# Kernel tuning notes

Measured on AMD Instinct MI355X. Metric: run time of the kernel, lower is better.

## Reference

```python
import jax, jax.numpy as jnp
import numpy as np

N_NODES = 100000
N_EDGES = 600000
D_IN = 128
D_OUT = 128


def setup_inputs() -> dict:
    key = jax.random.key(0)
    ks = jax.random.split(key, 8)
    stdv = 1.0 / np.sqrt(D_OUT)
    return {
        "x": jax.random.normal(ks[0], (N_NODES, D_IN), dtype=jnp.float32),
        "edge_src": jax.random.randint(ks[1], (N_EDGES,), 0, N_NODES, dtype=jnp.int32),
        "edge_dst": jax.random.randint(ks[2], (N_EDGES,), 0, N_NODES, dtype=jnp.int32),
        "edge_weight": jax.random.uniform(ks[3], (N_EDGES,), dtype=jnp.float32),
        "weight_l": jax.random.uniform(ks[4], (D_IN, D_OUT), minval=-stdv, maxval=stdv, dtype=jnp.float32),
        "bias_l": jax.random.uniform(ks[5], (D_OUT,), minval=-stdv, maxval=stdv, dtype=jnp.float32),
        "weight_r": jax.random.uniform(ks[6], (D_IN, D_OUT), minval=-stdv, maxval=stdv, dtype=jnp.float32),
        "bias_r": jax.random.uniform(ks[7], (D_OUT,), minval=-stdv, maxval=stdv, dtype=jnp.float32),
    }


def reference(x, edge_src, edge_dst, edge_weight, weight_l, bias_l, weight_r, bias_r):
    # h = input @ weight_l  -> [N, D_OUT]
    h = x @ weight_l
    # spmm(adj, h): out[dst] += adj[dst, src] * h[src]
    msgs = h[edge_src] * edge_weight[:, None]          # [E, D_OUT] gather
    agg = jax.ops.segment_sum(msgs, edge_dst, num_segments=N_NODES)
    out = agg + bias_l
    # root_weight branch (size is None)
    out = out + x @ weight_r + bias_r
    return out
```

## Files before the change

kernel.cpp:

```cpp
#include <hip/hip_runtime.h>
#include <hip/hip_bf16.h>

#define D 128
#define SCAN_BLK 256
#define SCAN_VPT 4
#define SCAN_TILE (SCAN_BLK * SCAN_VPT)

typedef __attribute__((ext_vector_type(8))) short short8;
typedef __attribute__((ext_vector_type(4))) float f32x4;

__global__ __launch_bounds__(256) void prep_w(
    const float* __restrict__ Wl, const float* __restrict__ Wr,
    const float* __restrict__ bl, const float* __restrict__ br,
    __hip_bfloat16* __restrict__ WTl, __hip_bfloat16* __restrict__ WTr,
    float* __restrict__ bsum) {
  const int tid = blockIdx.x * 256 + threadIdx.x;
  const int n = (tid >> 7) & 127;
  const int k = tid & 127;
  if (tid < 16384) {
    WTl[n * D + k] = __float2bfloat16(Wl[k * D + n]);
  } else {
    WTr[n * D + k] = __float2bfloat16(Wr[k * D + n]);
  }
  if (tid < 128) bsum[tid] = bl[tid] + br[tid];
}

__global__ __launch_bounds__(256) void gemm_mfma(
    const float* __restrict__ x,
    const __hip_bfloat16* __restrict__ WTl,
    const __hip_bfloat16* __restrict__ WTr,
    const float* __restrict__ bsum,
    __hip_bfloat16* __restrict__ h,
    float* __restrict__ out,
    int n_rowtiles) {
  __shared__ __hip_bfloat16 xs[16][136];
  const int t = threadIdx.x;
  const int wave = t >> 6;
  const int lane = t & 63;
  const int m = lane & 15;
  const int q = lane >> 4;

  const __hip_bfloat16* __restrict__ WT = (wave < 2) ? WTl : WTr;
  const int ctbase = (wave & 1) * 4;
  short8 bfrag[4][4];
#pragma unroll
  for (int ct = 0; ct < 4; ++ct) {
    const int n0 = (ctbase + ct) * 16;
#pragma unroll
    for (int ks = 0; ks < 4; ++ks)
      bfrag[ct][ks] = *(const short8*)&WT[(n0 + m) * D + ks * 32 + q * 8];
  }

  const int srow = t >> 4;
  const int scol = (t & 15) * 8;

  for (int rt = blockIdx.x; rt < n_rowtiles; rt += gridDim.x) {
    const int rowbase = rt * 16;
    {
      const float4* src = (const float4*)&x[(size_t)(rowbase + srow) * D + scol];
      const float4 v0 = src[0], v1 = src[1];
      __hip_bfloat16* dst = &xs[srow][scol];
      dst[0] = __float2bfloat16(v0.x); dst[1] = __float2bfloat16(v0.y);
      dst[2] = __float2bfloat16(v0.z); dst[3] = __float2bfloat16(v0.w);
      dst[4] = __float2bfloat16(v1.x); dst[5] = __float2bfloat16(v1.y);
      dst[6] = __float2bfloat16(v1.z); dst[7] = __float2bfloat16(v1.w);
    }
    __syncthreads();

    f32x4 acc[4];
#pragma unroll
    for (int ct = 0; ct < 4; ++ct)
#pragma unroll
      for (int r = 0; r < 4; ++r) acc[ct][r] = 0.f;

#pragma unroll
    for (int ks = 0; ks < 4; ++ks) {
      const short8 afrag = *(const short8*)&xs[m][ks * 32 + q * 8];
#pragma unroll
      for (int ct = 0; ct < 4; ++ct)
        acc[ct] = __builtin_amdgcn_mfma_f32_16x16x32_bf16(afrag, bfrag[ct][ks], acc[ct], 0, 0, 0);
    }

    if (wave < 2) {
#pragma unroll
      for (int ct = 0; ct < 4; ++ct) {
        const int n = (ctbase + ct) * 16 + m;
#pragma unroll
        for (int r = 0; r < 4; ++r)
          h[(size_t)(rowbase + q * 4 + r) * D + n] = __float2bfloat16(acc[ct][r]);
      }
    } else {
#pragma unroll
      for (int ct = 0; ct < 4; ++ct) {
        const int n = (ctbase + ct) * 16 + m;
        const float b = bsum[n];
#pragma unroll
        for (int r = 0; r < 4; ++r)
          out[(size_t)(rowbase + q * 4 + r) * D + n] = acc[ct][r] + b;
      }
    }
    __syncthreads();
  }
}

__global__ __launch_bounds__(256) void hist_kernel(
    const int* __restrict__ edst, int* __restrict__ deg, int n_edges) {
  const int e = blockIdx.x * 256 + threadIdx.x;
  if (e < n_edges) atomicAdd(&deg[edst[e]], 1);
}

__global__ __launch_bounds__(SCAN_BLK) void scan1_kernel(
    const int* __restrict__ deg, int* __restrict__ offsets,
    int* __restrict__ partials, int n) {
  __shared__ int sdata[SCAN_BLK];
  const int t = threadIdx.x;
  const int base = blockIdx.x * SCAN_TILE + t * SCAN_VPT;

  int v[SCAN_VPT];
  int s = 0;
#pragma unroll
  for (int j = 0; j < SCAN_VPT; ++j) {
    v[j] = (base + j < n) ? deg[base + j] : 0;
    s += v[j];
  }
  sdata[t] = s;
  __syncthreads();
  for (int off = 1; off < SCAN_BLK; off <<= 1) {
    int xv = (t >= off) ? sdata[t - off] : 0;
    __syncthreads();
    sdata[t] += xv;
    __syncthreads();
  }
  int excl = sdata[t] - s;
  if (t == SCAN_BLK - 1) partials[blockIdx.x] = sdata[t];
  int run = excl;
#pragma unroll
  for (int j = 0; j < SCAN_VPT; ++j) {
    if (base + j < n) offsets[base + j] = run;
    run += v[j];
  }
}

__global__ __launch_bounds__(128) void scan2_kernel(int* __restrict__ partials, int nparts) {
  __shared__ int sd[128];
  const int t = threadIdx.x;
  const int v = (t < nparts) ? partials[t] : 0;
  sd[t] = v;
  __syncthreads();
  for (int off = 1; off < 128; off <<= 1) {
    int xv = (t >= off) ? sd[t - off] : 0;
    __syncthreads();
    sd[t] += xv;
    __syncthreads();
  }
  if (t < nparts) partials[t] = sd[t] - v;
}

__global__ __launch_bounds__(SCAN_BLK) void scan3_kernel(
    int* __restrict__ offsets, int* __restrict__ pos,
    const int* __restrict__ partials, int n, int n_edges) {
  const int base = blockIdx.x * SCAN_TILE + threadIdx.x * SCAN_VPT;
  const int add = partials[blockIdx.x];
#pragma unroll
  for (int j = 0; j < SCAN_VPT; ++j) {
    const int i = base + j;
    if (i < n) {
      const int o = offsets[i] + add;
      offsets[i] = o;
      pos[i] = o;
    }
  }
  if (blockIdx.x == 0 && threadIdx.x == 0) offsets[n] = n_edges;
}

__global__ __launch_bounds__(256) void scatter_kernel(
    const int* __restrict__ esrc, const int* __restrict__ edst,
    const float* __restrict__ ew, int* __restrict__ pos,
    int2* __restrict__ pairs, int n_edges) {
  const int e = blockIdx.x * 256 + threadIdx.x;
  if (e >= n_edges) return;
  const int d = edst[e];
  const int slot = atomicAdd(&pos[d], 1);
  pairs[slot] = make_int2(esrc[e], __float_as_int(ew[e]));
}

__global__ __launch_bounds__(256) void aggregate_kernel(
    const __hip_bfloat16* __restrict__ h, const int* __restrict__ offsets,
    const int2* __restrict__ pairs, float* __restrict__ out, int n_nodes) {
  const int node = blockIdx.x * 4 + (threadIdx.x >> 6);
  if (node >= n_nodes) return;
  const int t = threadIdx.x & 63;
  const int begin = offsets[node];
  const int end = offsets[node + 1];
  const __hip_bfloat162* __restrict__ h2 = (const __hip_bfloat162*)h;

  float2 acc = *(const float2*)&out[(size_t)node * D + 2 * t];

  int i = begin;
  for (; i + 4 <= end; i += 4) {
    const int2 p0 = pairs[i + 0];
    const int2 p1 = pairs[i + 1];
    const int2 p2 = pairs[i + 2];
    const int2 p3 = pairs[i + 3];
    const __hip_bfloat162 a0 = h2[(size_t)p0.x * (D / 2) + t];
    const __hip_bfloat162 a1 = h2[(size_t)p1.x * (D / 2) + t];
    const __hip_bfloat162 a2 = h2[(size_t)p2.x * (D / 2) + t];
    const __hip_bfloat162 a3 = h2[(size_t)p3.x * (D / 2) + t];
    const float w0 = __int_as_float(p0.y), w1 = __int_as_float(p1.y);
    const float w2 = __int_as_float(p2.y), w3 = __int_as_float(p3.y);
    acc.x = fmaf(w0, __bfloat162float(a0.x), acc.x);
    acc.y = fmaf(w0, __bfloat162float(a0.y), acc.y);
    acc.x = fmaf(w1, __bfloat162float(a1.x), acc.x);
    acc.y = fmaf(w1, __bfloat162float(a1.y), acc.y);
    acc.x = fmaf(w2, __bfloat162float(a2.x), acc.x);
    acc.y = fmaf(w2, __bfloat162float(a2.y), acc.y);
    acc.x = fmaf(w3, __bfloat162float(a3.x), acc.x);
    acc.y = fmaf(w3, __bfloat162float(a3.y), acc.y);
  }
  for (; i < end; ++i) {
    const int2 p = pairs[i];
    const __hip_bfloat162 a = h2[(size_t)p.x * (D / 2) + t];
    const float w = __int_as_float(p.y);
    acc.x = fmaf(w, __bfloat162float(a.x), acc.x);
    acc.y = fmaf(w, __bfloat162float(a.y), acc.y);
  }
  *(float2*)&out[(size_t)node * D + 2 * t] = acc;
}

extern "C" void kernel_launch(void* const* d_in, const int* in_sizes, int n_in,
                              void* d_out, int out_size, void* d_ws, size_t ws_size,
                              hipStream_t stream) {
  const float* x   = (const float*)d_in[0];
  const int* esrc  = (const int*)d_in[1];
  const int* edst  = (const int*)d_in[2];
  const float* ew  = (const float*)d_in[3];
  const float* Wl  = (const float*)d_in[4];
  const float* bl  = (const float*)d_in[5];
  const float* Wr  = (const float*)d_in[6];
  const float* br  = (const float*)d_in[7];
  float* out = (float*)d_out;

  const int n_nodes = in_sizes[0] / D;
  const int n_edges = in_sizes[1];

  char* ws = (char*)d_ws;
  size_t off = 0;
  __hip_bfloat16* h = (__hip_bfloat16*)(ws + off);
  off += (size_t)n_nodes * D * sizeof(__hip_bfloat16);
  off = (off + 15) & ~15ull;
  int* offsets = (int*)(ws + off);
  off += (size_t)(n_nodes + 1) * sizeof(int);
  off = (off + 15) & ~15ull;
  int* pos = (int*)(ws + off);
  off += (size_t)n_nodes * sizeof(int);
  off = (off + 15) & ~15ull;
  int* partials = (int*)(ws + off);
  off += 1024 * sizeof(int);
  off = (off + 15) & ~15ull;
  int2* pairs = (int2*)(ws + off);
  off += (size_t)n_edges * sizeof(int2);
  off = (off + 15) & ~15ull;
  __hip_bfloat16* WTl = (__hip_bfloat16*)(ws + off);
  off += (size_t)D * D * sizeof(__hip_bfloat16);
  __hip_bfloat16* WTr = (__hip_bfloat16*)(ws + off);
  off += (size_t)D * D * sizeof(__hip_bfloat16);
  float* bsum = (float*)(ws + off);
  off += D * sizeof(float);

  prep_w<<<128, 256, 0, stream>>>(Wl, Wr, bl, br, WTl, WTr, bsum);
  const int n_rowtiles = (n_nodes + 15) / 16;
  const int gemm_grid = n_rowtiles < 2048 ? n_rowtiles : 2048;
  gemm_mfma<<<gemm_grid, 256, 0, stream>>>(x, WTl, WTr, bsum, h, out, n_rowtiles);

  hipMemsetAsync(pos, 0, (size_t)n_nodes * sizeof(int), stream);
  hist_kernel<<<(n_edges + 255) / 256, 256, 0, stream>>>(edst, pos, n_edges);
  const int nparts = (n_nodes + SCAN_TILE - 1) / SCAN_TILE;
  scan1_kernel<<<nparts, SCAN_BLK, 0, stream>>>(pos, offsets, partials, n_nodes);
  scan2_kernel<<<1, 128, 0, stream>>>(partials, nparts);
  scan3_kernel<<<nparts, SCAN_BLK, 0, stream>>>(offsets, pos, partials, n_nodes, n_edges);
  scatter_kernel<<<(n_edges + 255) / 256, 256, 0, stream>>>(esrc, edst, ew, pos, pairs, n_edges);

  aggregate_kernel<<<(n_nodes + 3) / 4, 256, 0, stream>>>(h, offsets, pairs, out, n_nodes);
}
```

Before: 251.0 us.

## Fuse histogram into h GEMM, root GEMM into aggregation, drop scan2

Runs the degree histogram inside the h GEMM kernel and drops the separate hist launch. The root-weight GEMM plus bias moves into the aggregation kernel, which stages it in shared memory, so out is written once instead of written then re-read and rewritten. scan2 is removed by having each scan3 block reduce its preceding partials itself. This saves launches and an N×D fp32 round trip, but the aggregation kernel now uses more shared memory, re-reads x, and assigns four nodes per wave sequentially, which may cut latency hiding. sage_out also has no bounds check, so it assumes n_nodes is a multiple of 16.

```diff
diff --git a/kernel.cpp b/kernel.cpp
--- a/kernel.cpp
+++ b/kernel.cpp
@@ -25,14 +25,15 @@
   if (tid < 128) bsum[tid] = bl[tid] + br[tid];
 }
 
-__global__ __launch_bounds__(256) void gemm_mfma(
-    const float* __restrict__ x,
-    const __hip_bfloat16* __restrict__ WTl,
-    const __hip_bfloat16* __restrict__ WTr,
-    const float* __restrict__ bsum,
+__global__ __launch_bounds__(256) void gemm_h(
+    const float* __restrict__ x, const __hip_bfloat16* __restrict__ WTl,
     __hip_bfloat16* __restrict__ h,
-    float* __restrict__ out,
+    const int* __restrict__ edst, int* __restrict__ deg, int n_edges,
     int n_rowtiles) {
+  const int gsz = gridDim.x * 256;
+  for (int e = blockIdx.x * 256 + threadIdx.x; e < n_edges; e += gsz)
+    atomicAdd(&deg[edst[e]], 1);
+
   __shared__ __hip_bfloat16 xs[16][136];
   const int t = threadIdx.x;
   const int wave = t >> 6;
@@ -40,15 +41,13 @@
   const int m = lane & 15;
   const int q = lane >> 4;
 
-  const __hip_bfloat16* __restrict__ WT = (wave < 2) ? WTl : WTr;
-  const int ctbase = (wave & 1) * 4;
-  short8 bfrag[4][4];
-#pragma unroll
-  for (int ct = 0; ct < 4; ++ct) {
-    const int n0 = (ctbase + ct) * 16;
+  short8 bfrag[2][4];
+#pragma unroll
+  for (int c = 0; c < 2; ++c) {
+    const int n0 = wave * 32 + c * 16;
 #pragma unroll
     for (int ks = 0; ks < 4; ++ks)
-      bfrag[ct][ks] = *(const short8*)&WT[(n0 + m) * D + ks * 32 + q * 8];
+      bfrag[c][ks] = *(const short8*)&WTl[(n0 + m) * D + ks * 32 + q * 8];
   }
 
   const int srow = t >> 4;
@@ -67,46 +66,29 @@
     }
     __syncthreads();
 
-    f32x4 acc[4];
-#pragma unroll
-    for (int ct = 0; ct < 4; ++ct)
-#pragma unroll
-      for (int r = 0; r < 4; ++r) acc[ct][r] = 0.f;
+    f32x4 acc[2];
+#pragma unroll
+    for (int c = 0; c < 2; ++c)
+#pragma unroll
+      for (int r = 0; r < 4; ++r) acc[c][r] = 0.f;
 
 #pragma unroll
     for (int ks = 0; ks < 4; ++ks) {
       const short8 afrag = *(const short8*)&xs[m][ks * 32 + q * 8];
 #pragma unroll
-      for (int ct = 0; ct < 4; ++ct)
-        acc[ct] = __builtin_amdgcn_mfma_f32_16x16x32_bf16(afrag, bfrag[ct][ks], acc[ct], 0, 0, 0);
-    }
-
-    if (wave < 2) {
-#pragma unroll
-      for (int ct = 0; ct < 4; ++ct) {
-        const int n = (ctbase + ct) * 16 + m;
-#pragma unroll
-        for (int r = 0; r < 4; ++r)
-          h[(size_t)(rowbase + q * 4 + r) * D + n] = __float2bfloat16(acc[ct][r]);
-      }
-    } else {
-#pragma unroll
-      for (int ct = 0; ct < 4; ++ct) {
-        const int n = (ctbase + ct) * 16 + m;
-        const float b = bsum[n];
-#pragma unroll
-        for (int r = 0; r < 4; ++r)
-          out[(size_t)(rowbase + q * 4 + r) * D + n] = acc[ct][r] + b;
-      }
+      for (int c = 0; c < 2; ++c)
+        acc[c] = __builtin_amdgcn_mfma_f32_16x16x32_bf16(afrag, bfrag[c][ks], acc[c], 0, 0, 0);
+    }
+
+#pragma unroll
+    for (int c = 0; c < 2; ++c) {
+      const int n = wave * 32 + c * 16 + m;
+#pragma unroll
+      for (int r = 0; r < 4; ++r)
+        h[(size_t)(rowbase + q * 4 + r) * D + n] = __float2bfloat16(acc[c][r]);
     }
     __syncthreads();
   }
-}
-
-__global__ __launch_bounds__(256) void hist_kernel(
-    const int* __restrict__ edst, int* __restrict__ deg, int n_edges) {
-  const int e = blockIdx.x * 256 + threadIdx.x;
-  if (e < n_edges) atomicAdd(&deg[edst[e]], 1);
 }
 
 __global__ __launch_bounds__(SCAN_BLK) void scan1_kernel(
@@ -141,26 +123,21 @@
   }
 }
 
-__global__ __launch_bounds__(128) void scan2_kernel(int* __restrict__ partials, int nparts) {
-  __shared__ int sd[128];
-  const int t = threadIdx.x;
-  const int v = (t < nparts) ? partials[t] : 0;
-  sd[t] = v;
-  __syncthreads();
-  for (int off = 1; off < 128; off <<= 1) {
-    int xv = (t >= off) ? sd[t - off] : 0;
-    __syncthreads();
-    sd[t] += xv;
-    __syncthreads();
-  }
-  if (t < nparts) partials[t] = sd[t] - v;
-}
-
 __global__ __launch_bounds__(SCAN_BLK) void scan3_kernel(
     int* __restrict__ offsets, int* __restrict__ pos,
     const int* __restrict__ partials, int n, int n_edges) {
-  const int base = blockIdx.x * SCAN_TILE + threadIdx.x * SCAN_VPT;
-  const int add = partials[blockIdx.x];
+  __shared__ int s_add;
+  const int t = threadIdx.x;
+  if (t < 64) {
+    int v = 0;
+    for (int j = t; j < blockIdx.x; j += 64) v += partials[j];
+#pragma unroll
+    for (int off = 32; off > 0; off >>= 1) v += __shfl_down(v, off);
+    if (t == 0) s_add = v;
+  }
+  __syncthreads();
+  const int add = s_add;
+  const int base = blockIdx.x * SCAN_TILE + t * SCAN_VPT;
 #pragma unroll
   for (int j = 0; j < SCAN_VPT; ++j) {
     const int i = base + j;
@@ -170,7 +147,7 @@
       pos[i] = o;
     }
   }
-  if (blockIdx.x == 0 && threadIdx.x == 0) offsets[n] = n_edges;
+  if (blockIdx.x == 0 && t == 0) offsets[n] = n_edges;
 }
 
 __global__ __launch_bounds__(256) void scatter_kernel(
@@ -184,47 +161,106 @@
   pairs[slot] = make_int2(esrc[e], __float_as_int(ew[e]));
 }
 
-__global__ __launch_bounds__(256) void aggregate_kernel(
-    const __hip_bfloat16* __restrict__ h, const int* __restrict__ offsets,
-    const int2* __restrict__ pairs, float* __restrict__ out, int n_nodes) {
-  const int node = blockIdx.x * 4 + (threadIdx.x >> 6);
-  if (node >= n_nodes) return;
-  const int t = threadIdx.x & 63;
-  const int begin = offsets[node];
-  const int end = offsets[node + 1];
+__global__ __launch_bounds__(256) void sage_out(
+    const float* __restrict__ x, const __hip_bfloat16* __restrict__ WTr,
+    const float* __restrict__ bsum, const __hip_bfloat16* __restrict__ h,
+    const int* __restrict__ offsets, const int2* __restrict__ pairs,
+    float* __restrict__ out) {
+  __shared__ __hip_bfloat16 xs[16][136];
+  __shared__ float ot[16][D];
+  const int t = threadIdx.x;
+  const int wave = t >> 6;
+  const int lane = t & 63;
+  const int m = lane & 15;
+  const int q = lane >> 4;
+  const int rowbase = blockIdx.x * 16;
+
+  short8 bfrag[2][4];
+#pragma unroll
+  for (int c = 0; c < 2; ++c) {
+    const int n0 = wave * 32 + c * 16;
+#pragma unroll
+    for (int ks = 0; ks < 4; ++ks)
+      bfrag[c][ks] = *(const short8*)&WTr[(n0 + m) * D + ks * 32 + q * 8];
+  }
+
+  {
+    const int srow = t >> 4;
+    const int scol = (t & 15) * 8;
+    const float4* src = (const float4*)&x[(size_t)(rowbase + srow) * D + scol];
+    const float4 v0 = src[0], v1 = src[1];
+    __hip_bfloat16* dst = &xs[srow][scol];
+    dst[0] = __float2bfloat16(v0.x); dst[1] = __float2bfloat16(v0.y);
+    dst[2] = __float2bfloat16(v0.z); dst[3] = __float2bfloat16(v0.w);
+    dst[4] = __float2bfloat16(v1.x); dst[5] = __float2bfloat16(v1.y);
+    dst[6] = __float2bfloat16(v1.z); dst[7] = __float2bfloat16(v1.w);
+  }
+  __syncthreads();
+
+  f32x4 acc[2];
+#pragma unroll
+  for (int c = 0; c < 2; ++c)
+#pragma unroll
+    for (int r = 0; r < 4; ++r) acc[c][r] = 0.f;
+
+#pragma unroll
+  for (int ks = 0; ks < 4; ++ks) {
+    const short8 afrag = *(const short8*)&xs[m][ks * 32 + q * 8];
+#pragma unroll
+    for (int c = 0; c < 2; ++c)
+      acc[c] = __builtin_amdgcn_mfma_f32_16x16x32_bf16(afrag, bfrag[c][ks], acc[c], 0, 0, 0);
+  }
+
+#pragma unroll
+  for (int c = 0; c < 2; ++c) {
+    const int n = wave * 32 + c * 16 + m;
+    const float b = bsum[n];
+#pragma unroll
+    for (int r = 0; r < 4; ++r)
+      ot[q * 4 + r][n] = acc[c][r] + b;
+  }
+  __syncthreads();
+
   const __hip_bfloat162* __restrict__ h2 = (const __hip_bfloat162*)h;
-
-  float2 acc = *(const float2*)&out[(size_t)node * D + 2 * t];
-
-  int i = begin;
-  for (; i + 4 <= end; i += 4) {
-    const int2 p0 = pairs[i + 0];
-    const int2 p1 = pairs[i + 1];
-    const int2 p2 = pairs[i + 2];
-    const int2 p3 = pairs[i + 3];
-    const __hip_bfloat162 a0 = h2[(size_t)p0.x * (D / 2) + t];
-    const __hip_bfloat162 a1 = h2[(size_t)p1.x * (D / 2) + t];
-    const __hip_bfloat162 a2 = h2[(size_t)p2.x * (D / 2) + t];
-    const __hip_bfloat162 a3 = h2[(size_t)p3.x * (D / 2) + t];
-    const float w0 = __int_as_float(p0.y), w1 = __int_as_float(p1.y);
-    const float w2 = __int_as_float(p2.y), w3 = __int_as_float(p3.y);
-    acc.x = fmaf(w0, __bfloat162float(a0.x), acc.x);
-    acc.y = fmaf(w0, __bfloat162float(a0.y), acc.y);
-    acc.x = fmaf(w1, __bfloat162float(a1.x), acc.x);
-    acc.y = fmaf(w1, __bfloat162float(a1.y), acc.y);
-    acc.x = fmaf(w2, __bfloat162float(a2.x), acc.x);
-    acc.y = fmaf(w2, __bfloat162float(a2.y), acc.y);
-    acc.x = fmaf(w3, __bfloat162float(a3.x), acc.x);
-    acc.y = fmaf(w3, __bfloat162float(a3.y), acc.y);
-  }
-  for (; i < end; ++i) {
-    const int2 p = pairs[i];
-    const __hip_bfloat162 a = h2[(size_t)p.x * (D / 2) + t];
-    const float w = __int_as_float(p.y);
-    acc.x = fmaf(w, __bfloat162float(a.x), acc.x);
-    acc.y = fmaf(w, __bfloat162float(a.y), acc.y);
-  }
-  *(float2*)&out[(size_t)node * D + 2 * t] = acc;
+#pragma unroll
+  for (int j = 0; j < 4; ++j) {
+    const int ln = wave * 4 + j;
+    const int node = rowbase + ln;
+    const int begin = offsets[node];
+    const int end = offsets[node + 1];
+
+    float2 a = *(const float2*)&ot[ln][2 * lane];
+
+    int i = begin;
+    for (; i + 4 <= end; i += 4) {
+      const int2 p0 = pairs[i + 0];
+      const int2 p1 = pairs[i + 1];
+      const int2 p2 = pairs[i + 2];
+      const int2 p3 = pairs[i + 3];
+      const __hip_bfloat162 a0 = h2[(size_t)p0.x * (D / 2) + lane];
+      const __hip_bfloat162 a1 = h2[(size_t)p1.x * (D / 2) + lane];
+      const __hip_bfloat162 a2 = h2[(size_t)p2.x * (D / 2) + lane];
+      const __hip_bfloat162 a3 = h2[(size_t)p3.x * (D / 2) + lane];
+      const float w0 = __int_as_float(p0.y), w1 = __int_as_float(p1.y);
+      const float w2 = __int_as_float(p2.y), w3 = __int_as_float(p3.y);
+      a.x = fmaf(w0, __bfloat162float(a0.x), a.x);
+      a.y = fmaf(w0, __bfloat162float(a0.y), a.y);
+      a.x = fmaf(w1, __bfloat162float(a1.x), a.x);
+      a.y = fmaf(w1, __bfloat162float(a1.y), a.y);
+      a.x = fmaf(w2, __bfloat162float(a2.x), a.x);
+      a.y = fmaf(w2, __bfloat162float(a2.y), a.y);
+      a.x = fmaf(w3, __bfloat162float(a3.x), a.x);
+      a.y = fmaf(w3, __bfloat162float(a3.y), a.y);
+    }
+    for (; i < end; ++i) {
+      const int2 p = pairs[i];
+      const __hip_bfloat162 av = h2[(size_t)p.x * (D / 2) + lane];
+      const float w = __int_as_float(p.y);
+      a.x = fmaf(w, __bfloat162float(av.x), a.x);
+      a.y = fmaf(w, __bfloat162float(av.y), a.y);
+    }
+    *(float2*)&out[(size_t)node * D + 2 * lane] = a;
+  }
 }
 
 extern "C" void kernel_launch(void* const* d_in, const int* in_sizes, int n_in,
@@ -267,18 +303,18 @@
   float* bsum = (float*)(ws + off);
   off += D * sizeof(float);
 
+  const int n_rowtiles = (n_nodes + 15) / 16;
+
+  hipMemsetAsync(pos, 0, (size_t)n_nodes * sizeof(int), stream);
   prep_w<<<128, 256, 0, stream>>>(Wl, Wr, bl, br, WTl, WTr, bsum);
-  const int n_rowtiles = (n_nodes + 15) / 16;
+
   const int gemm_grid = n_rowtiles < 2048 ? n_rowtiles : 2048;
-  gemm_mfma<<<gemm_grid, 256, 0, stream>>>(x, WTl, WTr, bsum, h, out, n_rowtiles);
-
-  hipMemsetAsync(pos, 0, (size_t)n_nodes * sizeof(int), stream);
-  hist_kernel<<<(n_edges + 255) / 256, 256, 0, stream>>>(edst, pos, n_edges);
+  gemm_h<<<gemm_grid, 256, 0, stream>>>(x, WTl, h, edst, pos, n_edges, n_rowtiles);
+
   const int nparts = (n_nodes + SCAN_TILE - 1) / SCAN_TILE;
   scan1_kernel<<<nparts, SCAN_BLK, 0, stream>>>(pos, offsets, partials, n_nodes);
-  scan2_kernel<<<1, 128, 0, stream>>>(partials, nparts);
   scan3_kernel<<<nparts, SCAN_BLK, 0, stream>>>(offsets, pos, partials, n_nodes, n_edges);
   scatter_kernel<<<(n_edges + 255) / 256, 256, 0, stream>>>(esrc, edst, ew, pos, pairs, n_edges);
 
-  aggregate_kernel<<<(n_nodes + 3) / 4, 256, 0, stream>>>(h, offsets, pairs, out, n_nodes);
-}
+  sage_out<<<n_rowtiles, 256, 0, stream>>>(x, WTr, bsum, h, offsets, pairs, out);
+}
```

New measurement: 236.8 us. 1.06x faster.
